# Kernel tuning notes

Hardware: AMD Instinct MI355X
Metric: run time of the kernel (lower is better)

Reference implementation:

```python
import jax, jax.numpy as jnp
import numpy as np
from jax import lax

T, D_IN, D_OUT = 8192, 4096, 4096
N_ADAPT, RANK = 8, 16


def setup_inputs() -> dict:
    key = jax.random.key(0)
    ks = jax.random.split(key, 6)
    x = jax.random.normal(ks[0], (T, D_IN), jnp.float32)
    weight_indices = jax.random.randint(ks[1], (T,), 0, N_ADAPT, jnp.int64 if jax.config.jax_enable_x64 else jnp.int32)
    W_base = jax.random.normal(ks[2], (D_OUT, D_IN), jnp.float32) * 0.02
    A_buffer = jax.random.normal(ks[3], (N_ADAPT, D_IN, RANK), jnp.float32) * 0.02
    B_buffer = jax.random.normal(ks[4], (N_ADAPT, RANK, D_OUT), jnp.float32) * 0.02
    DeltaW = jax.random.normal(ks[5], (N_ADAPT, D_IN, D_OUT), jnp.float32) * 0.02
    return {"x": x, "weight_indices": weight_indices, "W_base": W_base,
            "A_buffer": A_buffer, "B_buffer": B_buffer, "DeltaW": DeltaW}


def _ldmm(indices, x, A, B, D):
    """Per-token adapter matmul: out[t] = x[t] @ (DeltaW[j] + A[j] @ B[j]), j = indices[t].
    Grouped by adapter via masked GEMMs (fixed small adapter count), jit-friendly."""
    n_adapt = A.shape[0]
    acc0 = jnp.zeros((x.shape[0], D.shape[2]), x.dtype)

    def body(acc, inp):
        a_id, A_a, B_a, D_a = inp
        mask = (indices == a_id)[:, None]
        xm = jnp.where(mask, x, jnp.zeros((), x.dtype))  # [T, in]
        W_eff = D_a + A_a @ B_a                          # [in, out]
        return acc + xm @ W_eff, None

    acc, _ = lax.scan(body, acc0, (jnp.arange(n_adapt), A, B, D))
    return acc


def reference(x, weight_indices, W_base, A_buffer, B_buffer, DeltaW):
    base = x @ W_base.T                                   # ColumnParallelLinear
    delta = _ldmm(weight_indices, x, A_buffer, B_buffer, DeltaW)
    # NOTE: source has `base_output = +output` (unary plus, likely a typo for `+=`);
    # we implement the intended fused semantics base + ldmm.
    return base + delta
```

## Files before the change

### kernel.cpp

```cpp
#include <hip/hip_runtime.h>


#define T_TOKENS 8192
#define DIM 4096
#define NADAPT 8
#define RANK 16

#define BM2 256
#define GRIDX2 512

#define BM1 128
#define MAXT1 72

typedef __attribute__((ext_vector_type(8))) short bf16x8;
typedef __attribute__((ext_vector_type(4))) float f32x4;

__device__ __forceinline__ unsigned short f2bf(float f) {
  union { float f; unsigned u; } v; v.f = f;
  unsigned r = v.u + 0x7FFFu + ((v.u >> 16) & 1u);
  return (unsigned short)(r >> 16);
}

__device__ __forceinline__ void gload_lds16(const void* g, void* l) {
  __builtin_amdgcn_global_load_lds(
      (const __attribute__((address_space(1))) void*)g,
      (__attribute__((address_space(3))) void*)l, 16, 0, 0);
}

template <int N> __device__ __forceinline__ void vmwait() {
  if constexpr (N == 0)      asm volatile("s_waitcnt vmcnt(0)" ::: "memory");
  else if constexpr (N == 4) asm volatile("s_waitcnt vmcnt(4)" ::: "memory");
  else if constexpr (N == 8) asm volatile("s_waitcnt vmcnt(8)" ::: "memory");
}

__global__ void prep_kernel(const int* __restrict__ idx, int* __restrict__ perm,
                            int* __restrict__ meta, int padm) {
  __shared__ int s_cnt[NADAPT];
  __shared__ int s_padoff[NADAPT + 1];
  __shared__ int s_wsum[16];
  const int tid = threadIdx.x;
  const int lane = tid & 63;
  const int wave = tid >> 6;

  if (tid < NADAPT) s_cnt[tid] = 0;
  __syncthreads();
  for (int t = tid; t < T_TOKENS; t += 1024) atomicAdd(&s_cnt[idx[t]], 1);
  __syncthreads();

  if (tid == 0) {
    int off = 0, nt = 0;
    for (int j = 0; j < NADAPT; ++j) {
      meta[j] = s_cnt[j];
      s_padoff[j] = off;
      const int c = s_cnt[j];
      const int ntj = (c + padm - 1) / padm;
      for (int i = 0; i < ntj; ++i) {
        meta[32 + 3 * nt + 0] = j;
        meta[32 + 3 * nt + 1] = off + i * padm;
        meta[32 + 3 * nt + 2] = min(padm, c - i * padm);
        ++nt;
      }
      off += ntj * padm;
    }
    s_padoff[NADAPT] = off;
    meta[17] = nt;
    for (int j = 0; j <= NADAPT; ++j) meta[8 + j] = s_padoff[j];
  }
  __syncthreads();

  const int total_pad = s_padoff[NADAPT];
  for (int t = tid; t < total_pad; t += 1024) perm[t] = -1;
  __syncthreads();

  for (int j = 0; j < NADAPT; ++j) {
    int base = s_padoff[j];
    for (int c0 = 0; c0 < T_TOKENS; c0 += 1024) {
      const int t = c0 + tid;
      const int flag = (idx[t] == j) ? 1 : 0;
      const unsigned long long bal = __ballot(flag);
      const int wpos = __popcll(bal & ((1ULL << lane) - 1ULL));
      if (lane == 0) s_wsum[wave] = __popcll(bal);
      __syncthreads();
      int woff = 0, ctot = 0;
      for (int w = 0; w < 16; ++w) {
        const int v = s_wsum[w];
        if (w < wave) woff += v;
        ctot += v;
      }
      if (flag) perm[base + woff + wpos] = t;
      base += ctot;
      __syncthreads();
    }
  }
}

__global__ __launch_bounds__(256) void zero_tail_kernel(
    const int* __restrict__ perm, const int* __restrict__ meta,
    float* __restrict__ out) {
  const int ntiles = meta[17];
  const int mt = 32 + (int)(blockIdx.x >> 1);
  if (mt >= ntiles) return;
  const int half = blockIdx.x & 1;
  const int pbase = meta[32 + 3 * mt + 1] + half * 128;
  const int row = threadIdx.x >> 1;
  const int c0 = blockIdx.y * 128 + (threadIdx.x & 1) * 64;
  const int pr = perm[pbase + row];
  if (pr < 0) return;
  float4* p = (float4*)(out + (size_t)pr * DIM + c0);
  const float4 z = {0.f, 0.f, 0.f, 0.f};
#pragma unroll
  for (int k = 0; k < 16; ++k) p[k] = z;
}

__global__ void convert_x_kernel(const float* __restrict__ x,
                                 unsigned short* __restrict__ xb) {
  const long long i = (long long)blockIdx.x * 256 + threadIdx.x;
  const float4* x4 = (const float4*)x;
  const float4 a = x4[2 * i];
  const float4 b = x4[2 * i + 1];
  uint4 o;
  o.x = (unsigned)f2bf(a.x) | ((unsigned)f2bf(a.y) << 16);
  o.y = (unsigned)f2bf(a.z) | ((unsigned)f2bf(a.w) << 16);
  o.z = (unsigned)f2bf(b.x) | ((unsigned)f2bf(b.y) << 16);
  o.w = (unsigned)f2bf(b.z) | ((unsigned)f2bf(b.w) << 16);
  ((uint4*)xb)[i] = o;
}

__global__ __launch_bounds__(256) void build_wtot_all_kernel(
    const float* __restrict__ Wb, const float* __restrict__ Am,
    const float* __restrict__ Bm, const float* __restrict__ DW,
    unsigned short* __restrict__ Wt) {
  const int i0 = blockIdx.x << 6;
  const int o0 = blockIdx.y << 6;
  __shared__ float Dl[2][64 * 64];
  __shared__ float Alt[2][16][68];
  __shared__ float Bl[2][16][68];
  const int tid = threadIdx.x;
  const int to = (tid >> 4) << 2;
  const int ti = (tid & 15) << 2;

  float4 wbr[4];
#pragma unroll
  for (int m = 0; m < 4; ++m)
    wbr[m] = *(const float4*)(Wb + (size_t)(o0 + to + m) * DIM + i0 + ti);

  const int di = tid >> 4;
  const int do4 = (tid & 15) << 2;
  const int ar_i = tid >> 2, ar_r4 = (tid & 3) << 2;
  const int br_r = tid >> 4, br_o4 = (tid & 15) << 2;

  float4 dwr[4], ar, brv;
  {
    const float* dwp = DW + (size_t)i0 * DIM + o0;
#pragma unroll
    for (int q = 0; q < 4; ++q)
      dwr[q] = *(const float4*)(dwp + (size_t)(q * 16 + di) * DIM + do4);
    ar = *(const float4*)(Am + ((size_t)(i0 + ar_i)) * RANK + ar_r4);
    brv = *(const float4*)(Bm + (size_t)br_r * DIM + o0 + br_o4);
  }
#pragma unroll
  for (int q = 0; q < 4; ++q) {
    const int i = q * 16 + di;
    const int iq = i >> 2, ie = i & 3;
#pragma unroll
    for (int k = 0; k < 4; ++k) {
      const int o = do4 + k;
      Dl[0][o * 64 + (((iq ^ (o & 15)) << 2) | ie)] = ((const float*)&dwr[q])[k];
    }
  }
#pragma unroll
  for (int k = 0; k < 4; ++k) Alt[0][ar_r4 + k][ar_i] = ((const float*)&ar)[k];
  *(float4*)&Bl[0][br_r][br_o4] = brv;
  __syncthreads();

  for (int j = 0; j < NADAPT; ++j) {
    const int pb = j & 1;
    if (j + 1 < NADAPT) {
      const float* dwp = DW + ((size_t)(j + 1) * DIM + i0) * DIM + o0;
#pragma unroll
      for (int q = 0; q < 4; ++q)
        dwr[q] = *(const float4*)(dwp + (size_t)(q * 16 + di) * DIM + do4);
      ar = *(const float4*)(Am + ((size_t)(j + 1) * DIM + i0 + ar_i) * RANK + ar_r4);
      brv = *(const float4*)(Bm + ((size_t)(j + 1) * RANK + br_r) * DIM + o0 + br_o4);
    }
    float acc[4][4];
#pragma unroll
    for (int m = 0; m < 4; ++m) {
      const int o = to + m;
      const float4 d = *(const float4*)&Dl[pb][o * 64 + (((ti >> 2) ^ (o & 15)) << 2)];
      acc[m][0] = wbr[m].x + d.x; acc[m][1] = wbr[m].y + d.y;
      acc[m][2] = wbr[m].z + d.z; acc[m][3] = wbr[m].w + d.w;
    }
#pragma unroll
    for (int r = 0; r < RANK; ++r) {
      const float4 av = *(const float4*)&Alt[pb][r][ti];
      const float4 bv = *(const float4*)&Bl[pb][r][to];
#pragma unroll
      for (int m = 0; m < 4; ++m) {
        const float b = ((const float*)&bv)[m];
        acc[m][0] += b * av.x; acc[m][1] += b * av.y;
        acc[m][2] += b * av.z; acc[m][3] += b * av.w;
      }
    }
#pragma unroll
    for (int m = 0; m < 4; ++m) {
      const int o = to + m;
      const unsigned lo = (unsigned)f2bf(acc[m][0]) | ((unsigned)f2bf(acc[m][1]) << 16);
      const unsigned hi = (unsigned)f2bf(acc[m][2]) | ((unsigned)f2bf(acc[m][3]) << 16);
      uint2 pk; pk.x = lo; pk.y = hi;
      *(uint2*)(Wt + ((size_t)j * DIM + o0 + o) * DIM + i0 + ti) = pk;
    }
    if (j + 1 < NADAPT) {
      const int nb = pb ^ 1;
#pragma unroll
      for (int q = 0; q < 4; ++q) {
        const int i = q * 16 + di;
        const int iq = i >> 2, ie = i & 3;
#pragma unroll
        for (int k = 0; k < 4; ++k) {
          const int o = do4 + k;
          Dl[nb][o * 64 + (((iq ^ (o & 15)) << 2) | ie)] = ((const float*)&dwr[q])[k];
        }
      }
#pragma unroll
      for (int k = 0; k < 4; ++k) Alt[nb][ar_r4 + k][ar_i] = ((const float*)&ar)[k];
      *(float4*)&Bl[nb][br_r][br_o4] = brv;
      __syncthreads();
    }
  }
}

__global__ __launch_bounds__(256) void build_wtot_kernel(
    const float* __restrict__ Wb, const float* __restrict__ Am,
    const float* __restrict__ Bm, const float* __restrict__ DW,
    unsigned short* __restrict__ Wt, int j0) {
  const int jj = blockIdx.z;
  const int j = j0 + jj;
  const int i0 = blockIdx.x << 6;
  const int o0 = blockIdx.y << 6;
  __shared__ float Dl[64 * 64];
  __shared__ float Alt[16][68];
  __shared__ float Bl[16][68];
  const int tid = threadIdx.x;

  const float* dwp = DW + ((size_t)j * DIM + i0) * DIM + o0;
#pragma unroll
  for (int q = 0; q < 4; ++q) {
    const int lin = q * 256 + tid;
    const int i = lin >> 4;
    const int o4 = (lin & 15) << 2;
    const float4 v = *(const float4*)(dwp + (size_t)i * DIM + o4);
    const int iq = i >> 2, ie = i & 3;
#pragma unroll
    for (int k = 0; k < 4; ++k) {
      const int o = o4 + k;
      Dl[o * 64 + (((iq ^ (o & 15)) << 2) | ie)] = ((const float*)&v)[k];
    }
  }
  {
    const int ai = tid >> 2, r4 = (tid & 3) << 2;
    const float4 v = *(const float4*)(Am + ((size_t)j * DIM + i0 + ai) * RANK + r4);
#pragma unroll
    for (int k = 0; k < 4; ++k) Alt[r4 + k][ai] = ((const float*)&v)[k];
  }
  {
    const int br = tid >> 4, bo4 = (tid & 15) << 2;
    const float4 v = *(const float4*)(Bm + ((size_t)j * RANK + br) * DIM + o0 + bo4);
    *(float4*)&Bl[br][bo4] = v;
  }
  __syncthreads();

  const int to = (tid >> 4) << 2;
  const int ti = (tid & 15) << 2;
  float acc[4][4];

#pragma unroll
  for (int m = 0; m < 4; ++m) {
    const int o = to + m;
    const float4 w = *(const float4*)(Wb + (size_t)(o0 + o) * DIM + i0 + ti);
    const float4 d = *(const float4*)&Dl[o * 64 + (((ti >> 2) ^ (o & 15)) << 2)];
    acc[m][0] = w.x + d.x; acc[m][1] = w.y + d.y;
    acc[m][2] = w.z + d.z; acc[m][3] = w.w + d.w;
  }
#pragma unroll
  for (int r = 0; r < RANK; ++r) {
    const float4 av = *(const float4*)&Alt[r][ti];
    const float4 bv = *(const float4*)&Bl[r][to];
#pragma unroll
    for (int m = 0; m < 4; ++m) {
      const float b = ((const float*)&bv)[m];
      acc[m][0] += b * av.x; acc[m][1] += b * av.y;
      acc[m][2] += b * av.z; acc[m][3] += b * av.w;
    }
  }
#pragma unroll
  for (int m = 0; m < 4; ++m) {
    const int o = to + m;
    const unsigned lo = (unsigned)f2bf(acc[m][0]) | ((unsigned)f2bf(acc[m][1]) << 16);
    const unsigned hi = (unsigned)f2bf(acc[m][2]) | ((unsigned)f2bf(acc[m][3]) << 16);
    uint2 pk; pk.x = lo; pk.y = hi;
    *(uint2*)(Wt + ((size_t)jj * DIM + o0 + o) * DIM + i0 + ti) = pk;
  }
}

template <int BUF, int KK, int MQ, int VME, int SGRP, int SOP, int SKH, bool DOST>
__device__ __forceinline__ void do_phase(
    char* smem, int tid, int stile,
    const unsigned short* const* aB, const unsigned short* const* bB,
    const int* aoff, const int* boff, bf16x8* bfr, f32x4 (*acc)[4]) {
  const int grp = (BUF * 2 + KK) * 16384;
  if constexpr (MQ == 0) {
#pragma unroll
    for (int n = 0; n < 4; ++n)
      bfr[n] = *(const bf16x8*)(smem + 65536 + grp + boff[n]);
  }
  bf16x8 afr[4];
#pragma unroll
  for (int i = 0; i < 4; ++i)
    afr[i] = *(const bf16x8*)(smem + grp + aoff[MQ * 4 + i]);
  if constexpr (DOST) {
    const unsigned short* const* bs = SOP ? bB : aB;
#pragma unroll
    for (int q = 0; q < 2; ++q)
      gload_lds16(bs[q] + stile * 64 + SKH * 32,
                  smem + SOP * 65536 + SGRP * 16384 + q * 8192 + tid * 16);
  }
  __builtin_amdgcn_s_barrier();
  asm volatile("s_waitcnt lgkmcnt(0)" ::: "memory");
  __builtin_amdgcn_s_setprio(1);
#pragma unroll
  for (int i = 0; i < 4; ++i)
#pragma unroll
    for (int n = 0; n < 4; ++n)
      acc[MQ * 4 + i][n] =
          __builtin_amdgcn_mfma_f32_16x16x32_bf16(afr[i], bfr[n], acc[MQ * 4 + i][n], 0, 0, 0);
  __builtin_amdgcn_s_setprio(0);
  vmwait<VME>();
  __builtin_amdgcn_s_barrier();
}

template <int SGRP, int SOP, int SKH>
__device__ __forceinline__ void do_stage(
    char* smem, int tid, int stile,
    const unsigned short* const* aB, const unsigned short* const* bB) {
  const unsigned short* const* bs = SOP ? bB : aB;
#pragma unroll
  for (int q = 0; q < 2; ++q)
    gload_lds16(bs[q] + stile * 64 + SKH * 32,
                smem + SOP * 65536 + SGRP * 16384 + q * 8192 + tid * 16);
}

template <int NTILES, bool TAILK>
__global__ __launch_bounds__(512, 2) void gemm8_kernel(
    const unsigned short* __restrict__ xb, const unsigned short* __restrict__ Wt,
    const int* __restrict__ perm, const int* __restrict__ meta,
    float* __restrict__ out) {
  extern __shared__ char smem[];
  const int ntiles = meta[17];
  const int flat = blockIdx.x;
  int mt, nt, kc;
  if (TAILK) {
    kc = flat >> 7;
    const int r = flat & 127;
    mt = 32 + (r >> 4);
    nt = r & 15;
  } else {
    const int swz = (flat & 7) * (GRIDX2 / 8) + (flat >> 3);
    mt = swz >> 4;
    nt = swz & 15;
    kc = 0;
  }
  if (mt >= ntiles) return;
  const int adapter = meta[32 + 3 * mt];
  const int pbase = meta[32 + 3 * mt + 1];
  const int nbase = nt << 8;
  const size_t kbase = (size_t)kc * (NTILES * 64);

  const int tid = threadIdx.x;
  const int lane = tid & 63;
  const int wave = tid >> 6;
  const int wr = wave >> 2, wc = wave & 3;
  const int fr = lane & 15, kg = lane >> 4;

  int aoff[8], boff[4];
#pragma unroll
  for (int m = 0; m < 8; ++m) {
    const int row = wr * 128 + m * 16 + fr;
    const int r = row >> 1, hf = row & 1;
    const int c = ((hf << 2) | kg) ^ (r & 7);
    aoff[m] = r * 128 + c * 16;
  }
#pragma unroll
  for (int n = 0; n < 4; ++n) {
    const int row = wc * 64 + n * 16 + fr;
    const int r = row >> 1, hf = row & 1;
    const int c = ((hf << 2) | kg) ^ (r & 7);
    boff[n] = r * 128 + c * 16;
  }

  const unsigned short* aB[2];
  const unsigned short* bB[2];
#pragma unroll
  for (int q = 0; q < 2; ++q) {
    const int L = q * 512 + tid;
    const int r = L >> 3, c = L & 7;
    const int s = c ^ (r & 7);
    const int grow = 2 * r + (s >> 2);
    const int gk = (s & 3) << 3;
    int pr = perm[pbase + grow];
    if (pr < 0) pr = 0;
    aB[q] = xb + (size_t)pr * DIM + gk + kbase;
    bB[q] = Wt + ((size_t)adapter * DIM + nbase + grow) * DIM + gk + kbase;
  }

  const f32x4 zero = {0.f, 0.f, 0.f, 0.f};
  f32x4 acc[8][4];
#pragma unroll
  for (int m = 0; m < 8; ++m)
#pragma unroll
    for (int n = 0; n < 4; ++n) acc[m][n] = zero;
  bf16x8 bfr[4];

  do_stage<0, 0, 0>(smem, tid, 0, aB, bB);
  do_stage<0, 1, 0>(smem, tid, 0, aB, bB);
  do_stage<1, 0, 1>(smem, tid, 0, aB, bB);
  do_stage<1, 1, 1>(smem, tid, 0, aB, bB);
  do_stage<2, 0, 0>(smem, tid, 1, aB, bB);
  do_stage<2, 1, 0>(smem, tid, 1, aB, bB);
  vmwait<8>();
  __builtin_amdgcn_s_barrier();

  for (int it = 0; it < NTILES / 2 - 1; ++it) {
    const int t1 = 2 * it + 1, t2 = 2 * it + 2, t3 = 2 * it + 3;
    do_phase<0, 0, 0, -1, 3, 0, 1, true>(smem, tid, t1, aB, bB, aoff, boff, bfr, acc);
    do_phase<0, 0, 1,  8, 3, 1, 1, true>(smem, tid, t1, aB, bB, aoff, boff, bfr, acc);
    do_phase<0, 1, 0, -1, 0, 0, 0, true>(smem, tid, t2, aB, bB, aoff, boff, bfr, acc);
    do_phase<0, 1, 1,  8, 0, 1, 0, true>(smem, tid, t2, aB, bB, aoff, boff, bfr, acc);
    do_phase<1, 0, 0, -1, 1, 0, 1, true>(smem, tid, t2, aB, bB, aoff, boff, bfr, acc);
    do_phase<1, 0, 1,  8, 1, 1, 1, true>(smem, tid, t2, aB, bB, aoff, boff, bfr, acc);
    do_phase<1, 1, 0, -1, 2, 0, 0, true>(smem, tid, t3, aB, bB, aoff, boff, bfr, acc);
    do_phase<1, 1, 1,  8, 2, 1, 0, true>(smem, tid, t3, aB, bB, aoff, boff, bfr, acc);
  }
  do_phase<0, 0, 0, -1, 3, 0, 1, true >(smem, tid, NTILES - 1, aB, bB, aoff, boff, bfr, acc);
  do_phase<0, 0, 1,  8, 3, 1, 1, true >(smem, tid, NTILES - 1, aB, bB, aoff, boff, bfr, acc);
  do_phase<0, 1, 0, -1, 0, 0, 0, false>(smem, tid, 0, aB, bB, aoff, boff, bfr, acc);
  do_phase<0, 1, 1,  4, 0, 0, 0, false>(smem, tid, 0, aB, bB, aoff, boff, bfr, acc);
  do_phase<1, 0, 0, -1, 0, 0, 0, false>(smem, tid, 0, aB, bB, aoff, boff, bfr, acc);
  do_phase<1, 0, 1,  0, 0, 0, 0, false>(smem, tid, 0, aB, bB, aoff, boff, bfr, acc);
  do_phase<1, 1, 0, -1, 0, 0, 0, false>(smem, tid, 0, aB, bB, aoff, boff, bfr, acc);
  do_phase<1, 1, 1, -1, 0, 0, 0, false>(smem, tid, 0, aB, bB, aoff, boff, bfr, acc);

#pragma unroll
  for (int m = 0; m < 8; ++m) {
#pragma unroll
    for (int t = 0; t < 4; ++t) {
      const int rt = wr * 128 + m * 16 + kg * 4 + t;
      const int pr = perm[pbase + rt];
      if (pr < 0) continue;
      float* orow = out + (size_t)pr * DIM + nbase + wc * 64;
#pragma unroll
      for (int n = 0; n < 4; ++n) {
        if (TAILK) atomicAdd(&orow[n * 16 + fr], acc[m][n][t]);
        else       orow[n * 16 + fr] = acc[m][n][t];
      }
    }
  }
}

template <bool USE_XB>
__global__ __launch_bounds__(256) void gemm_kernel(
    const unsigned short* __restrict__ xb, const float* __restrict__ xf,
    const unsigned short* __restrict__ Wt,
    const int* __restrict__ perm, const int* __restrict__ meta,
    float* __restrict__ out, int j0, int npp) {
  const int ntiles = meta[17];
  const int mt = blockIdx.x;
  if (mt >= ntiles) return;
  const int adapter = meta[32 + 3 * mt];
  if (adapter < j0 || adapter >= j0 + npp) return;
  const int slot = adapter - j0;
  const int nt = blockIdx.y;
  const int pbase = meta[32 + 3 * mt + 1];
  const int nbase = nt << 7;

  __shared__ __align__(16) unsigned short As[BM1 * 64];
  __shared__ __align__(16) unsigned short Bs[BM1 * 64];

  const int tid = threadIdx.x;
  const int lane = tid & 63;
  const int wave = tid >> 6;

  const unsigned short* aSrcB[4];
  const float* aSrcF[4];
  const unsigned short* bSrc[4];
  unsigned short* aDst[4];
  unsigned short* bDst[4];
#pragma unroll
  for (int q = 0; q < 4; ++q) {
    const int c = wave * 4 + q;
    const int r = c * 8 + (lane >> 3);
    int pr = perm[pbase + r];
    if (pr < 0) pr = 0;
    if (USE_XB) aSrcB[q] = xb + (size_t)pr * DIM + (lane & 7) * 8;
    else        aSrcF[q] = xf + (size_t)pr * DIM + (lane & 7) * 8;
    bSrc[q] = Wt + ((size_t)slot * DIM + nbase + r) * DIM + (lane & 7) * 8;
    aDst[q] = As + c * 512;
    bDst[q] = Bs + c * 512;
  }

  const int wr = wave >> 1, wc = wave & 1;
  const int fr = lane & 15, kg = lane >> 4;

  const f32x4 zero = {0.f, 0.f, 0.f, 0.f};
  f32x4 acc[4][4];
#pragma unroll
  for (int m = 0; m < 4; ++m)
#pragma unroll
    for (int n = 0; n < 4; ++n) acc[m][n] = zero;

  for (int k0 = 0; k0 < DIM; k0 += 64) {
    if (USE_XB) {
#pragma unroll
      for (int q = 0; q < 4; ++q) gload_lds16(aSrcB[q] + k0, aDst[q]);
    } else {
#pragma unroll
      for (int q = 0; q < 4; ++q) {
        const float4 va = *(const float4*)(aSrcF[q] + k0);
        const float4 vb = *(const float4*)(aSrcF[q] + k0 + 4);
        union { bf16x8 v; unsigned short s[8]; } u;
        u.s[0] = f2bf(va.x); u.s[1] = f2bf(va.y); u.s[2] = f2bf(va.z); u.s[3] = f2bf(va.w);
        u.s[4] = f2bf(vb.x); u.s[5] = f2bf(vb.y); u.s[6] = f2bf(vb.z); u.s[7] = f2bf(vb.w);
        *(bf16x8*)(aDst[q] + lane * 8) = u.v;
      }
    }
#pragma unroll
    for (int q = 0; q < 4; ++q) gload_lds16(bSrc[q] + k0, bDst[q]);
    __syncthreads();
#pragma unroll
    for (int kk = 0; kk < 2; ++kk) {
      bf16x8 a[4], b[4];
#pragma unroll
      for (int m = 0; m < 4; ++m)
        a[m] = *(const bf16x8*)(&As[(wr * 64 + m * 16 + fr) * 64 + kk * 32 + kg * 8]);
#pragma unroll
      for (int n = 0; n < 4; ++n)
        b[n] = *(const bf16x8*)(&Bs[(wc * 64 + n * 16 + fr) * 64 + kk * 32 + kg * 8]);
#pragma unroll
      for (int m = 0; m < 4; ++m)
#pragma unroll
        for (int n = 0; n < 4; ++n)
          acc[m][n] = __builtin_amdgcn_mfma_f32_16x16x32_bf16(a[m], b[n], acc[m][n], 0, 0, 0);
    }
    __syncthreads();
  }

#pragma unroll
  for (int m = 0; m < 4; ++m) {
#pragma unroll
    for (int t = 0; t < 4; ++t) {
      const int rt = wr * 64 + m * 16 + kg * 4 + t;
      const int pr = perm[pbase + rt];
      if (pr < 0) continue;
      float* orow = out + (size_t)pr * DIM + nbase + wc * 64;
#pragma unroll
      for (int n = 0; n < 4; ++n) orow[n * 16 + fr] = acc[m][n][t];
    }
  }
}

extern "C" void kernel_launch(void* const* d_in, const int* in_sizes, int n_in,
                              void* d_out, int out_size, void* d_ws, size_t ws_size,
                              hipStream_t stream) {
  const float* x  = (const float*)d_in[0];
  const int* widx = (const int*)d_in[1];
  const float* Wb = (const float*)d_in[2];
  const float* Am = (const float*)d_in[3];
  const float* Bm = (const float*)d_in[4];
  const float* DW = (const float*)d_in[5];
  float* out = (float*)d_out;

  const size_t XB_BYTES = (size_t)T_TOKENS * DIM * 2;
  const size_t WT1_BYTES = (size_t)DIM * DIM * 2;
  const size_t PM_BYTES = 16384 * sizeof(int) + 4096;

  int npp = 0;
  bool use_xb = true;
  for (int cand = NADAPT; cand >= 1; cand >>= 1) {
    if (XB_BYTES + (size_t)cand * WT1_BYTES + PM_BYTES <= ws_size) { npp = cand; break; }
  }
  if (npp == 0) { npp = 1; use_xb = false; }

  bool use8 = (npp == NADAPT) &&
      (hipFuncSetAttribute((const void*)gemm8_kernel<64, false>,
                           hipFuncAttributeMaxDynamicSharedMemorySize, 131072) == hipSuccess) &&
      (hipFuncSetAttribute((const void*)gemm8_kernel<16, true>,
                           hipFuncAttributeMaxDynamicSharedMemorySize, 131072) == hipSuccess);

  char* ws = (char*)d_ws;
  unsigned short* xb = (unsigned short*)ws;
  unsigned short* Wt = (unsigned short*)(ws + (use_xb ? XB_BYTES : 0));
  char* tail = (char*)Wt + (size_t)npp * WT1_BYTES;
  int* perm = (int*)tail;
  int* meta = (int*)(tail + 16384 * sizeof(int));

  prep_kernel<<<dim3(1), dim3(1024), 0, stream>>>(widx, perm, meta, use8 ? BM2 : BM1);
  if (use_xb)
    convert_x_kernel<<<dim3(T_TOKENS * DIM / (256 * 8)), dim3(256), 0, stream>>>(x, xb);

  if (npp == NADAPT) {
    if (use8)
      zero_tail_kernel<<<dim3(16, DIM / 128), dim3(256), 0, stream>>>(perm, meta, out);
    build_wtot_all_kernel<<<dim3(DIM / 64, DIM / 64), dim3(256), 0, stream>>>(
        Wb, Am, Bm, DW, Wt);
    if (use8) {
      gemm8_kernel<64, false><<<dim3(GRIDX2), dim3(512), 131072, stream>>>(
          xb, Wt, perm, meta, out);
      gemm8_kernel<16, true><<<dim3(512), dim3(512), 131072, stream>>>(
          xb, Wt, perm, meta, out);
    } else {
      gemm_kernel<true><<<dim3(MAXT1, DIM / 128), dim3(256), 0, stream>>>(
          xb, nullptr, Wt, perm, meta, out, 0, NADAPT);
    }
  } else {
    const int passes = NADAPT / npp;
    for (int p = 0; p < passes; ++p) {
      const int j0 = p * npp;
      build_wtot_kernel<<<dim3(DIM / 64, DIM / 64, npp), dim3(256), 0, stream>>>(
          Wb, Am, Bm, DW, Wt, j0);
      if (use_xb)
        gemm_kernel<true><<<dim3(MAXT1, DIM / 128), dim3(256), 0, stream>>>(
            xb, nullptr, Wt, perm, meta, out, j0, npp);
      else
        gemm_kernel<false><<<dim3(MAXT1, DIM / 128), dim3(256), 0, stream>>>(
            nullptr, x, Wt, perm, meta, out, j0, npp);
    }
  }
}
```

Measured before the change: 629.0 us.

## Merge conversion with tail zeroing and fuse both GEMM launches into one grid

Folds the tail-zeroing work into the x-to-bf16 conversion kernel as extra blocks. It also merges the full-K GEMM and the split-K tail GEMM into a single launch, with the block index deciding the mode at runtime. Nontemporal loads and stores are added for streaming data (x, W_base, DeltaW, GEMM outputs) to reduce cache pollution. This cuts two launches and lets the tail split-K blocks overlap with the main tiles. The cost is that the K-loop trip count is now a runtime value rather than a template constant, which may hurt unrolling and scheduling.

```diff
diff --git a/kernel.cpp b/kernel.cpp
--- a/kernel.cpp
+++ b/kernel.cpp
@@ -7,7 +7,8 @@
 #define RANK 16
 
 #define BM2 256
-#define GRIDX2 512
+#define GRIDX1 512
+#define GRIDXALL 1024
 
 #define BM1 128
 #define MAXT1 72
@@ -94,36 +95,40 @@
   }
 }
 
-__global__ __launch_bounds__(256) void zero_tail_kernel(
-    const int* __restrict__ perm, const int* __restrict__ meta,
-    float* __restrict__ out) {
-  const int ntiles = meta[17];
-  const int mt = 32 + (int)(blockIdx.x >> 1);
-  if (mt >= ntiles) return;
-  const int half = blockIdx.x & 1;
-  const int pbase = meta[32 + 3 * mt + 1] + half * 128;
-  const int row = threadIdx.x >> 1;
-  const int c0 = blockIdx.y * 128 + (threadIdx.x & 1) * 64;
-  const int pr = perm[pbase + row];
-  if (pr < 0) return;
-  float4* p = (float4*)(out + (size_t)pr * DIM + c0);
-  const float4 z = {0.f, 0.f, 0.f, 0.f};
-#pragma unroll
-  for (int k = 0; k < 16; ++k) p[k] = z;
-}
-
-__global__ void convert_x_kernel(const float* __restrict__ x,
-                                 unsigned short* __restrict__ xb) {
-  const long long i = (long long)blockIdx.x * 256 + threadIdx.x;
-  const float4* x4 = (const float4*)x;
-  const float4 a = x4[2 * i];
-  const float4 b = x4[2 * i + 1];
-  uint4 o;
-  o.x = (unsigned)f2bf(a.x) | ((unsigned)f2bf(a.y) << 16);
-  o.y = (unsigned)f2bf(a.z) | ((unsigned)f2bf(a.w) << 16);
-  o.z = (unsigned)f2bf(b.x) | ((unsigned)f2bf(b.y) << 16);
-  o.w = (unsigned)f2bf(b.z) | ((unsigned)f2bf(b.w) << 16);
-  ((uint4*)xb)[i] = o;
+__global__ void convert_zero_kernel(const float* __restrict__ x,
+                                    unsigned short* __restrict__ xb,
+                                    const int* __restrict__ perm,
+                                    const int* __restrict__ meta,
+                                    float* __restrict__ out, int do_zero) {
+  const int tid = threadIdx.x;
+  if (blockIdx.x < 16384) {
+    const long long i = (long long)blockIdx.x * 256 + tid;
+    const f32x4* x4 = (const f32x4*)x;
+    const f32x4 a = __builtin_nontemporal_load(&x4[2 * i]);
+    const f32x4 b = __builtin_nontemporal_load(&x4[2 * i + 1]);
+    uint4 o;
+    o.x = (unsigned)f2bf(a.x) | ((unsigned)f2bf(a.y) << 16);
+    o.y = (unsigned)f2bf(a.z) | ((unsigned)f2bf(a.w) << 16);
+    o.z = (unsigned)f2bf(b.x) | ((unsigned)f2bf(b.y) << 16);
+    o.w = (unsigned)f2bf(b.z) | ((unsigned)f2bf(b.w) << 16);
+    ((uint4*)xb)[i] = o;
+  } else if (do_zero) {
+    const int b = blockIdx.x - 16384;
+    const int mth = b >> 5;
+    const int strip = b & 31;
+    const int ntiles = meta[17];
+    const int mt = 32 + (mth >> 1);
+    if (mt >= ntiles) return;
+    const int pbase = meta[32 + 3 * mt + 1] + (mth & 1) * 128;
+    const int row = tid >> 1;
+    const int c0 = strip * 128 + (tid & 1) * 64;
+    const int pr = perm[pbase + row];
+    if (pr < 0) return;
+    float4* p = (float4*)(out + (size_t)pr * DIM + c0);
+    const float4 z = {0.f, 0.f, 0.f, 0.f};
+#pragma unroll
+    for (int k = 0; k < 16; ++k) p[k] = z;
+  }
 }
 
 __global__ __launch_bounds__(256) void build_wtot_all_kernel(
@@ -139,22 +144,25 @@
   const int to = (tid >> 4) << 2;
   const int ti = (tid & 15) << 2;
 
-  float4 wbr[4];
+  f32x4 wbr[4];
 #pragma unroll
   for (int m = 0; m < 4; ++m)
-    wbr[m] = *(const float4*)(Wb + (size_t)(o0 + to + m) * DIM + i0 + ti);
+    wbr[m] = __builtin_nontemporal_load(
+        (const f32x4*)(Wb + (size_t)(o0 + to + m) * DIM + i0 + ti));
 
   const int di = tid >> 4;
   const int do4 = (tid & 15) << 2;
   const int ar_i = tid >> 2, ar_r4 = (tid & 3) << 2;
   const int br_r = tid >> 4, br_o4 = (tid & 15) << 2;
 
-  float4 dwr[4], ar, brv;
+  f32x4 dwr[4];
+  float4 ar, brv;
   {
     const float* dwp = DW + (size_t)i0 * DIM + o0;
 #pragma unroll
     for (int q = 0; q < 4; ++q)
-      dwr[q] = *(const float4*)(dwp + (size_t)(q * 16 + di) * DIM + do4);
+      dwr[q] = __builtin_nontemporal_load(
+          (const f32x4*)(dwp + (size_t)(q * 16 + di) * DIM + do4));
     ar = *(const float4*)(Am + ((size_t)(i0 + ar_i)) * RANK + ar_r4);
     brv = *(const float4*)(Bm + (size_t)br_r * DIM + o0 + br_o4);
   }
@@ -165,7 +173,7 @@
 #pragma unroll
     for (int k = 0; k < 4; ++k) {
       const int o = do4 + k;
-      Dl[0][o * 64 + (((iq ^ (o & 15)) << 2) | ie)] = ((const float*)&dwr[q])[k];
+      Dl[0][o * 64 + (((iq ^ (o & 15)) << 2) | ie)] = dwr[q][k];
     }
   }
 #pragma unroll
@@ -179,7 +187,8 @@
       const float* dwp = DW + ((size_t)(j + 1) * DIM + i0) * DIM + o0;
 #pragma unroll
       for (int q = 0; q < 4; ++q)
-        dwr[q] = *(const float4*)(dwp + (size_t)(q * 16 + di) * DIM + do4);
+        dwr[q] = __builtin_nontemporal_load(
+            (const f32x4*)(dwp + (size_t)(q * 16 + di) * DIM + do4));
       ar = *(const float4*)(Am + ((size_t)(j + 1) * DIM + i0 + ar_i) * RANK + ar_r4);
       brv = *(const float4*)(Bm + ((size_t)(j + 1) * RANK + br_r) * DIM + o0 + br_o4);
     }
@@ -219,7 +228,7 @@
 #pragma unroll
         for (int k = 0; k < 4; ++k) {
           const int o = do4 + k;
-          Dl[nb][o * 64 + (((iq ^ (o & 15)) << 2) | ie)] = ((const float*)&dwr[q])[k];
+          Dl[nb][o * 64 + (((iq ^ (o & 15)) << 2) | ie)] = dwr[q][k];
         }
       }
 #pragma unroll
@@ -350,31 +359,29 @@
                 smem + SOP * 65536 + SGRP * 16384 + q * 8192 + tid * 16);
 }
 
-template <int NTILES, bool TAILK>
-__global__ __launch_bounds__(512, 2) void gemm8_kernel(
+__global__ __launch_bounds__(512, 2) void gemm8_all_kernel(
     const unsigned short* __restrict__ xb, const unsigned short* __restrict__ Wt,
     const int* __restrict__ perm, const int* __restrict__ meta,
     float* __restrict__ out) {
   extern __shared__ char smem[];
   const int ntiles = meta[17];
   const int flat = blockIdx.x;
-  int mt, nt, kc;
-  if (TAILK) {
-    kc = flat >> 7;
-    const int r = flat & 127;
-    mt = 32 + (r >> 4);
-    nt = r & 15;
+  int mt, nt, kc, ntk;
+  bool tailk;
+  if (flat < GRIDX1) {
+    const int swz = (flat & 7) * (GRIDX1 / 8) + (flat >> 3);
+    mt = swz >> 4; nt = swz & 15; kc = 0; ntk = 64; tailk = false;
   } else {
-    const int swz = (flat & 7) * (GRIDX2 / 8) + (flat >> 3);
-    mt = swz >> 4;
-    nt = swz & 15;
-    kc = 0;
+    const int f = flat - GRIDX1;
+    kc = f >> 7;
+    const int r = f & 127;
+    mt = 32 + (r >> 4); nt = r & 15; ntk = 16; tailk = true;
   }
   if (mt >= ntiles) return;
   const int adapter = meta[32 + 3 * mt];
   const int pbase = meta[32 + 3 * mt + 1];
   const int nbase = nt << 8;
-  const size_t kbase = (size_t)kc * (NTILES * 64);
+  const size_t kbase = (size_t)kc * ((size_t)ntk * 64);
 
   const int tid = threadIdx.x;
   const int lane = tid & 63;
@@ -430,7 +437,7 @@
   vmwait<8>();
   __builtin_amdgcn_s_barrier();
 
-  for (int it = 0; it < NTILES / 2 - 1; ++it) {
+  for (int it = 0; it < ntk / 2 - 1; ++it) {
     const int t1 = 2 * it + 1, t2 = 2 * it + 2, t3 = 2 * it + 3;
     do_phase<0, 0, 0, -1, 3, 0, 1, true>(smem, tid, t1, aB, bB, aoff, boff, bfr, acc);
     do_phase<0, 0, 1,  8, 3, 1, 1, true>(smem, tid, t1, aB, bB, aoff, boff, bfr, acc);
@@ -441,8 +448,8 @@
     do_phase<1, 1, 0, -1, 2, 0, 0, true>(smem, tid, t3, aB, bB, aoff, boff, bfr, acc);
     do_phase<1, 1, 1,  8, 2, 1, 0, true>(smem, tid, t3, aB, bB, aoff, boff, bfr, acc);
   }
-  do_phase<0, 0, 0, -1, 3, 0, 1, true >(smem, tid, NTILES - 1, aB, bB, aoff, boff, bfr, acc);
-  do_phase<0, 0, 1,  8, 3, 1, 1, true >(smem, tid, NTILES - 1, aB, bB, aoff, boff, bfr, acc);
+  do_phase<0, 0, 0, -1, 3, 0, 1, true >(smem, tid, ntk - 1, aB, bB, aoff, boff, bfr, acc);
+  do_phase<0, 0, 1,  8, 3, 1, 1, true >(smem, tid, ntk - 1, aB, bB, aoff, boff, bfr, acc);
   do_phase<0, 1, 0, -1, 0, 0, 0, false>(smem, tid, 0, aB, bB, aoff, boff, bfr, acc);
   do_phase<0, 1, 1,  4, 0, 0, 0, false>(smem, tid, 0, aB, bB, aoff, boff, bfr, acc);
   do_phase<1, 0, 0, -1, 0, 0, 0, false>(smem, tid, 0, aB, bB, aoff, boff, bfr, acc);
@@ -460,8 +467,8 @@
       float* orow = out + (size_t)pr * DIM + nbase + wc * 64;
 #pragma unroll
       for (int n = 0; n < 4; ++n) {
-        if (TAILK) atomicAdd(&orow[n * 16 + fr], acc[m][n][t]);
-        else       orow[n * 16 + fr] = acc[m][n][t];
+        if (tailk) atomicAdd(&orow[n * 16 + fr], acc[m][n][t]);
+        else       __builtin_nontemporal_store(acc[m][n][t], &orow[n * 16 + fr]);
       }
     }
   }
@@ -591,9 +598,7 @@
   if (npp == 0) { npp = 1; use_xb = false; }
 
   bool use8 = (npp == NADAPT) &&
-      (hipFuncSetAttribute((const void*)gemm8_kernel<64, false>,
-                           hipFuncAttributeMaxDynamicSharedMemorySize, 131072) == hipSuccess) &&
-      (hipFuncSetAttribute((const void*)gemm8_kernel<16, true>,
+      (hipFuncSetAttribute((const void*)gemm8_all_kernel,
                            hipFuncAttributeMaxDynamicSharedMemorySize, 131072) == hipSuccess);
 
   char* ws = (char*)d_ws;
@@ -605,17 +610,14 @@
 
   prep_kernel<<<dim3(1), dim3(1024), 0, stream>>>(widx, perm, meta, use8 ? BM2 : BM1);
   if (use_xb)
-    convert_x_kernel<<<dim3(T_TOKENS * DIM / (256 * 8)), dim3(256), 0, stream>>>(x, xb);
+    convert_zero_kernel<<<dim3(16384 + 512), dim3(256), 0, stream>>>(
+        x, xb, perm, meta, out, use8 ? 1 : 0);
 
   if (npp == NADAPT) {
-    if (use8)
-      zero_tail_kernel<<<dim3(16, DIM / 128), dim3(256), 0, stream>>>(perm, meta, out);
     build_wtot_all_kernel<<<dim3(DIM / 64, DIM / 64), dim3(256), 0, stream>>>(
         Wb, Am, Bm, DW, Wt);
     if (use8) {
-      gemm8_kernel<64, false><<<dim3(GRIDX2), dim3(512), 131072, stream>>>(
-          xb, Wt, perm, meta, out);
-      gemm8_kernel<16, true><<<dim3(512), dim3(512), 131072, stream>>>(
+      gemm8_all_kernel<<<dim3(GRIDXALL), dim3(512), 131072, stream>>>(
           xb, Wt, perm, meta, out);
     } else {
       gemm_kernel<true><<<dim3(MAXT1, DIM / 128), dim3(256), 0, stream>>>(
```

Result: faster. 590.5 us (-6.1%).
